# Kernel optimization log

Measured on AMD Instinct MI355X. Metric: run time of the kernel, lower is better.

## Reference

```python
import jax, jax.numpy as jnp
import numpy as np

B, T, C = 2, 2048, 1024
H, D = 16, 64
EPS = 1e-05
SCALE = 1.0 / np.sqrt(D)


def _rmsnorm(x, w):
    # normalize over last dim (head_dim)
    return w * (x * jax.lax.rsqrt(jnp.mean(x * x, axis=-1, keepdims=True) + EPS))


def setup_inputs() -> dict:
    key = jax.random.key(0)
    ks = jax.random.split(key, 8)
    x = jax.random.normal(ks[0], (B, T, C), dtype=jnp.float32)
    # causal mask, 1 = attend, 0 = masked
    attention_mask = jnp.tril(jnp.ones((T, T), dtype=jnp.int32))[None, None]
    s = 1.0 / np.sqrt(C)
    Wq = jax.random.normal(ks[1], (C, H * D), dtype=jnp.float32) * s
    Wk = jax.random.normal(ks[2], (C, H * D), dtype=jnp.float32) * s
    Wv = jax.random.normal(ks[3], (C, H * D), dtype=jnp.float32) * s
    Wo = jax.random.normal(ks[4], (H * D, C), dtype=jnp.float32) * s
    q_norm_w = jnp.ones((D,), dtype=jnp.float32)
    k_norm_w = jnp.ones((D,), dtype=jnp.float32)
    gate = jnp.ones((1, H, 1, 1), dtype=jnp.float32)
    return {"x": x, "attention_mask": attention_mask, "Wq": Wq, "Wk": Wk,
            "Wv": Wv, "Wo": Wo, "q_norm_w": q_norm_w, "k_norm_w": k_norm_w,
            "gate": gate}


def reference(x, attention_mask, Wq, Wk, Wv, Wo, q_norm_w, k_norm_w, gate):
    Bx, Tx, Cx = x.shape
    vx = x @ Wv                                   # [B,T,H*D] (kept for value residual)
    q = (x @ Wq).reshape(Bx, Tx, H, D).transpose(0, 2, 1, 3)  # [B,H,T,D]
    k = (x @ Wk).reshape(Bx, Tx, H, D).transpose(0, 2, 1, 3)
    v = vx.reshape(Bx, Tx, H, D).transpose(0, 2, 1, 3)
    q = _rmsnorm(q, q_norm_w)
    k = _rmsnorm(k, k_norm_w)
    att = jnp.einsum('bhqd,bhkd->bhqk', q, k) * SCALE
    att = jnp.where(attention_mask == 0, -jnp.inf, att)
    att = jax.nn.softmax(att, axis=-1)
    att = att * gate                              # per-head gating after softmax
    out = jnp.einsum('bhqk,bhkd->bhqd', att, v)
    out = out.transpose(0, 2, 1, 3).reshape(Bx, Tx, Cx)
    out = out + vx                                # value residual
    out = out @ Wo
    return out
```

## Files before the change

kernel.cpp:

```cpp
#include <hip/hip_runtime.h>

#define T_SEQ 2048
#define CDIM 1024
#define NHEAD 16
#define HDIM 64
#define BATCH 2
#define EPSV 1e-5f
#define SCALE 0.125f
#define LOG2E 1.44269504088896f
#define SMAX 16.0f

typedef __attribute__((ext_vector_type(8))) short bf16x8;
typedef __attribute__((ext_vector_type(4))) float f32x4;

__device__ __forceinline__ float b2f(short s) {
  unsigned u = ((unsigned)(unsigned short)s) << 16;
  return __builtin_bit_cast(float, u);
}
__device__ __forceinline__ short f2b(float f) {
  unsigned u = __builtin_bit_cast(unsigned, f);
  unsigned r = (u + 0x7fffu + ((u >> 16) & 1u)) >> 16;
  return (short)r;
}
__device__ __forceinline__ unsigned cvt_pk_bf16(float a, float b) {
  unsigned r;
  asm("v_cvt_pk_bf16_f32 %0, %1, %2" : "=v"(r) : "v"(a), "v"(b));
  return r;
}

__device__ __forceinline__ void gld16(const void* g, void* l) {
  __builtin_amdgcn_global_load_lds((const __attribute__((address_space(1))) unsigned*)g,
                                   (__attribute__((address_space(3))) unsigned*)l, 16, 0, 0);
}

__device__ __forceinline__ void stage_sw(short* lds, const char* gbase, int gstride,
                                         int w, int l) {
#pragma unroll
  for (int i = 0; i < 2; ++i) {
    int chunk = w * 2048 + i * 1024 + l * 16;
    int row = chunk >> 7;
    int bir = chunk & 127;
    const char* src = gbase + (size_t)row * gstride + (bir ^ ((row & 7) << 4));
    gld16(src, (char*)lds + (w * 2048 + i * 1024));
  }
}

__global__ __launch_bounds__(256) void prep(const float* __restrict__ x,
                                            const float* __restrict__ Wq,
                                            const float* __restrict__ Wk,
                                            const float* __restrict__ Wv,
                                            const float* __restrict__ Wo,
                                            short* __restrict__ xb,
                                            short* __restrict__ WT) {
  __shared__ float tile[64][65];
  const int bid = blockIdx.x;
  if (bid < 2048) {
    size_t i = ((size_t)bid * 256 + threadIdx.x) * 8;
    float4 a = *(const float4*)&x[i];
    float4 b = *(const float4*)&x[i + 4];
    short4 lo, hi;
    lo.x = f2b(a.x); lo.y = f2b(a.y); lo.z = f2b(a.z); lo.w = f2b(a.w);
    hi.x = f2b(b.x); hi.y = f2b(b.y); hi.z = f2b(b.z); hi.w = f2b(b.w);
    *(short4*)&xb[i] = lo;
    *(short4*)&xb[i + 4] = hi;
    return;
  }
  const int t = bid - 2048;
  const int z = t >> 8, rem = t & 255;
  const float* W = (z == 0) ? Wq : (z == 1) ? Wk : (z == 2) ? Wv : Wo;
  const int r0 = (rem >> 4) * 64, c0 = (rem & 15) * 64;
  const int tr = threadIdx.x >> 4, tc4 = (threadIdx.x & 15) * 4;
#pragma unroll
  for (int i = 0; i < 4; ++i) {
    float4 v = *(const float4*)&W[(size_t)(r0 + tr + i * 16) * 1024 + c0 + tc4];
    tile[tr + i * 16][tc4 + 0] = v.x;
    tile[tr + i * 16][tc4 + 1] = v.y;
    tile[tr + i * 16][tc4 + 2] = v.z;
    tile[tr + i * 16][tc4 + 3] = v.w;
  }
  __syncthreads();
#pragma unroll
  for (int i = 0; i < 4; ++i) {
    int n = tr + i * 16;
    short4 o;
    o.x = f2b(tile[tc4 + 0][n]);
    o.y = f2b(tile[tc4 + 1][n]);
    o.z = f2b(tile[tc4 + 2][n]);
    o.w = f2b(tile[tc4 + 3][n]);
    *(short4*)&WT[((size_t)(z * 1024) + c0 + n) * 1024 + r0 + tc4] = o;
  }
}

template <int BN, bool F32OUT, bool NORM, bool VTOUT>
__global__ __launch_bounds__(256) void gemm_bf16(const short* __restrict__ A,
                                                 const short* __restrict__ Bt,
                                                 void* __restrict__ Cv,
                                                 const float* __restrict__ qw,
                                                 const float* __restrict__ kw,
                                                 short* __restrict__ VTb,
                                                 int M, int N, int K) {
  constexpr int NFR = BN / 32;
  __shared__ __attribute__((aligned(16))) short As[2][128 * 32];
  __shared__ __attribute__((aligned(16))) short Bs[2][BN * 32];
  const int tid = threadIdx.x;
  const int w = tid >> 6, l = tid & 63;
  const int g = l >> 4, c = l & 15;
  const int wm = w >> 1, wn = w & 1;
  const int m0 = blockIdx.y * 128, n0 = blockIdx.x * BN;
  const char* Ab = (const char*)A;
  const char* Bb = (const char*)Bt;

  auto stage = [&](int k0, int buf) {
#pragma unroll
    for (int i = 0; i < 2; ++i) {
      int chunk = w * 2048 + i * 1024 + l * 16;
      int row = chunk >> 6, bir = chunk & 63;
      gld16(Ab + ((size_t)(m0 + row) * K + k0) * 2 + bir,
            (char*)As[buf] + (w * 2048 + i * 1024));
    }
#pragma unroll
    for (int i = 0; i < BN / 64; ++i) {
      int chunk = w * (BN * 16) + i * 1024 + l * 16;
      int row = chunk >> 6, bir = chunk & 63;
      gld16(Bb + ((size_t)(n0 + row) * K + k0) * 2 + bir,
            (char*)Bs[buf] + (w * (BN * 16) + i * 1024));
    }
  };

  f32x4 acc[4][NFR];
#pragma unroll
  for (int mt = 0; mt < 4; ++mt)
#pragma unroll
    for (int nt = 0; nt < NFR; ++nt) {
      f32x4 z = {0.f, 0.f, 0.f, 0.f};
      acc[mt][nt] = z;
    }

  stage(0, 0);
  __syncthreads();
  int cur = 0;
  for (int k0 = 0; k0 < K; k0 += 32) {
    if (k0 + 32 < K) stage(k0 + 32, cur ^ 1);
    bf16x8 a[4], bf[NFR];
#pragma unroll
    for (int mt = 0; mt < 4; ++mt)
      a[mt] = *(const bf16x8*)&As[cur][(wm * 64 + mt * 16 + c) * 32 + g * 8];
#pragma unroll
    for (int nt = 0; nt < NFR; ++nt)
      bf[nt] = *(const bf16x8*)&Bs[cur][(wn * (BN / 2) + nt * 16 + c) * 32 + g * 8];
#pragma unroll
    for (int mt = 0; mt < 4; ++mt)
#pragma unroll
      for (int nt = 0; nt < NFR; ++nt)
        acc[mt][nt] = __builtin_amdgcn_mfma_f32_16x16x32_bf16(a[mt], bf[nt], acc[mt][nt], 0, 0, 0);
    __syncthreads();
    cur ^= 1;
  }

  if constexpr (NORM) {
    if (n0 < 2048) {
      const float* wgt = (n0 < 1024) ? qw : kw;
      const float scl = (n0 < 1024) ? SCALE * LOG2E : 1.f;
      float w4[NFR];
#pragma unroll
      for (int nt = 0; nt < NFR; ++nt) w4[nt] = wgt[nt * 16 + c] * scl;
#pragma unroll
      for (int mt = 0; mt < 4; ++mt)
#pragma unroll
        for (int r = 0; r < 4; ++r) {
          float s = 0.f;
#pragma unroll
          for (int nt = 0; nt < NFR; ++nt) s += acc[mt][nt][r] * acc[mt][nt][r];
          s += __shfl_xor(s, 1);
          s += __shfl_xor(s, 2);
          s += __shfl_xor(s, 4);
          s += __shfl_xor(s, 8);
          const float rstd = rsqrtf(s * (1.0f / 64.0f) + EPSV);
#pragma unroll
          for (int nt = 0; nt < NFR; ++nt) acc[mt][nt][r] *= rstd * w4[nt];
        }
    }
  }

  if constexpr (VTOUT) {
    if (n0 >= 2048) {
      const int bb = m0 >> 11;
      const int tbase = (m0 & 2047) + wm * 64 + 4 * g;
#pragma unroll
      for (int nt = 0; nt < NFR; ++nt) {
        const int cv = n0 - 2048 + wn * (BN / 2) + nt * 16 + c;
        short* dst = VTb + ((size_t)(bb * 1024 + cv)) * T_SEQ;
#pragma unroll
        for (int mt = 0; mt < 4; ++mt) {
          short4 o;
          o.x = f2b(acc[mt][nt][0]);
          o.y = f2b(acc[mt][nt][1]);
          o.z = f2b(acc[mt][nt][2]);
          o.w = f2b(acc[mt][nt][3]);
          *(short4*)&dst[tbase + mt * 16] = o;
        }
      }
    }
  }

  if constexpr (F32OUT) {
    float* C = (float*)Cv;
#pragma unroll
    for (int mt = 0; mt < 4; ++mt)
#pragma unroll
      for (int nt = 0; nt < NFR; ++nt)
#pragma unroll
        for (int r = 0; r < 4; ++r)
          C[(size_t)(m0 + wm * 64 + mt * 16 + 4 * g + r) * N + n0 + wn * (BN / 2) + nt * 16 + c] =
              acc[mt][nt][r];
  } else {
    short* C = (short*)Cv;
#pragma unroll
    for (int mt = 0; mt < 4; ++mt)
#pragma unroll
      for (int nt = 0; nt < NFR; ++nt)
#pragma unroll
        for (int r = 0; r < 4; ++r)
          C[(size_t)(m0 + wm * 64 + mt * 16 + 4 * g + r) * N + n0 + wn * (BN / 2) + nt * 16 + c] =
              f2b(acc[mt][nt][r]);
  }
}

__global__ __launch_bounds__(256) void attn_fwd(const short* __restrict__ QKV,
                                                const short* __restrict__ VT,
                                                const float* __restrict__ gate,
                                                short* __restrict__ Ob) {
  __shared__ __attribute__((aligned(16))) short pool[20480];
  short* Qs = pool;
  short* Ksb = pool + 4096;
  short* Vsb = pool + 12288;

  const int bid = blockIdx.x;
  const int xcd = bid & 7, s = bid >> 3;
  const int a = s & 31, bq = s >> 5, k4 = a >> 2;
  const int qt = (bq == 0) ? 31 - k4 : (bq == 1) ? k4 : (bq == 2) ? 23 - k4 : 8 + k4;
  const int bh = xcd * 4 + (a & 3);
  const int h = bh & 15, b = bh >> 4;
  const int q0 = qt * 64;
  const int tid = threadIdx.x;
  const int w = tid >> 6, l = tid & 63;
  const int g = l >> 4, c = l & 15;

  const char* qkb = (const char*)QKV;
  const char* kbase = qkb + ((size_t)(b * T_SEQ) * 3072 + 1024 + h * 64) * 2;
  const char* vtb = (const char*)VT + ((size_t)(b * NHEAD + h) * 64) * T_SEQ * 2;
  const float gh = gate[h];

  stage_sw(Qs, qkb + ((size_t)(b * T_SEQ + q0) * 3072 + h * 64) * 2, 3072 * 2, w, l);
  stage_sw(Ksb, kbase, 3072 * 2, w, l);
  stage_sw(Vsb, vtb, T_SEQ * 2, w, l);
  __syncthreads();

  bf16x8 qf[2];
  {
    const int row = w * 16 + c;
#pragma unroll
    for (int ks = 0; ks < 2; ++ks)
      qf[ks] = *(const bf16x8*)&Qs[row * 64 + ((ks * 32 + g * 8) ^ ((row & 7) << 3))];
  }
  short* ps = pool + (w << 10);

  f32x4 oacc[4];
#pragma unroll
  for (int dt = 0; dt < 4; ++dt) {
    f32x4 z = {0.f, 0.f, 0.f, 0.f};
    oacc[dt] = z;
  }
  float lpart = 0.f;
  int cur = 0;

  for (int kt = 0; kt <= qt; ++kt) {
    if (kt < qt) {
      stage_sw(Ksb + ((cur ^ 1) << 12), kbase + (size_t)(kt + 1) * 64 * 3072 * 2, 3072 * 2, w, l);
      stage_sw(Vsb + ((cur ^ 1) << 12), vtb + (size_t)(kt + 1) * 64 * 2, T_SEQ * 2, w, l);
    }
    f32x4 sacc[4];
#pragma unroll
    for (int mt = 0; mt < 4; ++mt) {
      f32x4 z = {-SMAX, -SMAX, -SMAX, -SMAX};
      sacc[mt] = z;
    }
    __builtin_amdgcn_s_setprio(1);
#pragma unroll
    for (int mt = 0; mt < 4; ++mt) {
      const int row = mt * 16 + c;
#pragma unroll
      for (int ks = 0; ks < 2; ++ks) {
        bf16x8 kf = *(const bf16x8*)&Ksb[(cur << 12) + row * 64 + ((ks * 32 + g * 8) ^ ((row & 7) << 3))];
        sacc[mt] = __builtin_amdgcn_mfma_f32_16x16x32_bf16(kf, qf[ks], sacc[mt], 0, 0, 0);
      }
    }
    __builtin_amdgcn_s_setprio(0);
    bf16x8 vf[4][2];
#pragma unroll
    for (int dt = 0; dt < 4; ++dt) {
      const int row = dt * 16 + c;
#pragma unroll
      for (int ks = 0; ks < 2; ++ks)
        vf[dt][ks] = *(const bf16x8*)&Vsb[(cur << 12) + row * 64 + ((ks * 32 + g * 8) ^ ((row & 7) << 3))];
    }
    if (kt == qt) {
#pragma unroll
      for (int mt = 0; mt < 4; ++mt)
#pragma unroll
        for (int r = 0; r < 4; ++r)
          if (mt * 16 + 4 * g + r > w * 16 + c) sacc[mt][r] = -1e30f;
    }
#pragma unroll
    for (int mt = 0; mt < 4; ++mt) {
      float p0 = exp2f(sacc[mt][0]);
      float p1 = exp2f(sacc[mt][1]);
      float p2 = exp2f(sacc[mt][2]);
      float p3 = exp2f(sacc[mt][3]);
      lpart += (p0 + p1) + (p2 + p3);
      uint2 pk;
      pk.x = cvt_pk_bf16(p0, p1);
      pk.y = cvt_pk_bf16(p2, p3);
      *(uint2*)&ps[(c << 6) + ((mt * 16 + 4 * g) ^ ((c & 7) << 3))] = pk;
    }
    bf16x8 pb[2];
#pragma unroll
    for (int ks = 0; ks < 2; ++ks)
      pb[ks] = *(const bf16x8*)&ps[(c << 6) + ((ks * 32 + g * 8) ^ ((c & 7) << 3))];
    __builtin_amdgcn_s_setprio(1);
#pragma unroll
    for (int dt = 0; dt < 4; ++dt)
#pragma unroll
      for (int ks = 0; ks < 2; ++ks)
        oacc[dt] = __builtin_amdgcn_mfma_f32_16x16x32_bf16(vf[dt][ks], pb[ks], oacc[dt], 0, 0, 0);
    __builtin_amdgcn_s_setprio(0);
    __syncthreads();
    cur ^= 1;
  }
  float lsum = lpart;
  lsum += __shfl_xor(lsum, 16);
  lsum += __shfl_xor(lsum, 32);
  const float gl = gh / lsum;
  const short* Vr = QKV + (size_t)(b * T_SEQ + q0 + w * 16 + c) * 3072 + 2048 + h * 64;
  short* Oro = Ob + (size_t)(b * T_SEQ + q0 + w * 16 + c) * 1024 + h * 64;
#pragma unroll
  for (int dt = 0; dt < 4; ++dt) {
    const int d0 = dt * 16 + 4 * g;
    short4 vres = *(const short4*)&Vr[d0];
    short4 o;
    o.x = f2b(oacc[dt][0] * gl + b2f(vres.x));
    o.y = f2b(oacc[dt][1] * gl + b2f(vres.y));
    o.z = f2b(oacc[dt][2] * gl + b2f(vres.z));
    o.w = f2b(oacc[dt][3] * gl + b2f(vres.w));
    *(short4*)&Oro[d0] = o;
  }
}

extern "C" void kernel_launch(void* const* d_in, const int* in_sizes, int n_in,
                              void* d_out, int out_size, void* d_ws, size_t ws_size,
                              hipStream_t stream) {
  const float* x  = (const float*)d_in[0];
  const float* Wq = (const float*)d_in[2];
  const float* Wk = (const float*)d_in[3];
  const float* Wv = (const float*)d_in[4];
  const float* Wo = (const float*)d_in[5];
  const float* qw = (const float*)d_in[6];
  const float* kw = (const float*)d_in[7];
  const float* gate = (const float*)d_in[8];
  float* out = (float*)d_out;

  char* ws = (char*)d_ws;
  short* xb  = (short*)ws;
  short* WT  = (short*)(ws + ((size_t)8 << 20));
  short* QKV = (short*)(ws + ((size_t)16 << 20));
  short* VTb = (short*)(ws + ((size_t)40 << 20));
  short* Obf = (short*)(ws + ((size_t)48 << 20));

  const int M = BATCH * T_SEQ;

  prep<<<3072, 256, 0, stream>>>(x, Wq, Wk, Wv, Wo, xb, WT);
  gemm_bf16<128, false, true, true><<<dim3(24, 32), 256, 0, stream>>>(
      xb, WT, QKV, qw, kw, VTb, M, 3072, CDIM);
  attn_fwd<<<1024, 256, 0, stream>>>(QKV, VTb, gate, Obf);
  gemm_bf16<128, true, false, false><<<dim3(8, 32), 256, 0, stream>>>(
      Obf, WT + (size_t)3072 * 1024, out, nullptr, nullptr, nullptr, M, CDIM, CDIM);
}
```

Measured before the change: 126.4 us.

## Triple-buffer GEMM with swizzled LDS, XCD-aware block remap, separate V transpose

The bf16 GEMM moves from double to triple buffering of LDS tiles, using vmcnt-based waits and one barrier per k-step so global loads run two tiles ahead. It adds an XOR swizzle to the LDS layout to reduce bank conflicts, remaps block IDs so neighbouring tiles land on the same XCD for better L2 reuse, and raises wave priority around the MFMA block. The fused transposed-V store in the QKV GEMM epilogue is replaced by a separate vt_kernel that transposes V through shared memory. That adds one launch and an extra read and write of V in exchange for a simpler epilogue with fewer scattered stores.

```diff
diff --git a/kernel.cpp b/kernel.cpp
--- a/kernel.cpp
+++ b/kernel.cpp
@@ -91,115 +91,112 @@
   }
 }
 
-template <int BN, bool F32OUT, bool NORM, bool VTOUT>
+template <bool F32OUT, bool NORM>
 __global__ __launch_bounds__(256) void gemm_bf16(const short* __restrict__ A,
                                                  const short* __restrict__ Bt,
                                                  void* __restrict__ Cv,
                                                  const float* __restrict__ qw,
                                                  const float* __restrict__ kw,
-                                                 short* __restrict__ VTb,
-                                                 int M, int N, int K) {
-  constexpr int NFR = BN / 32;
-  __shared__ __attribute__((aligned(16))) short As[2][128 * 32];
-  __shared__ __attribute__((aligned(16))) short Bs[2][BN * 32];
+                                                 int M, int N, int K, int nbx) {
+  __shared__ __attribute__((aligned(16))) short As[3][4096];
+  __shared__ __attribute__((aligned(16))) short Bs[3][4096];
   const int tid = threadIdx.x;
   const int w = tid >> 6, l = tid & 63;
   const int g = l >> 4, c = l & 15;
   const int wm = w >> 1, wn = w & 1;
-  const int m0 = blockIdx.y * 128, n0 = blockIdx.x * BN;
+  const int cpx = gridDim.x >> 3;
+  const int wg = (blockIdx.x & 7) * cpx + (blockIdx.x >> 3);
+  const int bx = wg % nbx, by = wg / nbx;
+  const int m0 = by * 128, n0 = bx * 128;
   const char* Ab = (const char*)A;
   const char* Bb = (const char*)Bt;
 
   auto stage = [&](int k0, int buf) {
 #pragma unroll
     for (int i = 0; i < 2; ++i) {
-      int chunk = w * 2048 + i * 1024 + l * 16;
-      int row = chunk >> 6, bir = chunk & 63;
-      gld16(Ab + ((size_t)(m0 + row) * K + k0) * 2 + bir,
+      int ci = w * 128 + i * 64 + l;
+      int row = ci >> 2, c4 = ci & 3;
+      gld16(Ab + ((size_t)(m0 + row) * K + k0) * 2 + ((c4 ^ (row & 3)) << 4),
             (char*)As[buf] + (w * 2048 + i * 1024));
     }
 #pragma unroll
-    for (int i = 0; i < BN / 64; ++i) {
-      int chunk = w * (BN * 16) + i * 1024 + l * 16;
-      int row = chunk >> 6, bir = chunk & 63;
-      gld16(Bb + ((size_t)(n0 + row) * K + k0) * 2 + bir,
-            (char*)Bs[buf] + (w * (BN * 16) + i * 1024));
+    for (int i = 0; i < 2; ++i) {
+      int ci = w * 128 + i * 64 + l;
+      int row = ci >> 2, c4 = ci & 3;
+      gld16(Bb + ((size_t)(n0 + row) * K + k0) * 2 + ((c4 ^ (row & 3)) << 4),
+            (char*)Bs[buf] + (w * 2048 + i * 1024));
     }
   };
 
-  f32x4 acc[4][NFR];
+  f32x4 acc[4][4];
 #pragma unroll
   for (int mt = 0; mt < 4; ++mt)
 #pragma unroll
-    for (int nt = 0; nt < NFR; ++nt) {
+    for (int nt = 0; nt < 4; ++nt) {
       f32x4 z = {0.f, 0.f, 0.f, 0.f};
       acc[mt][nt] = z;
     }
 
+  const int NT = K >> 5;
   stage(0, 0);
-  __syncthreads();
-  int cur = 0;
-  for (int k0 = 0; k0 < K; k0 += 32) {
-    if (k0 + 32 < K) stage(k0 + 32, cur ^ 1);
-    bf16x8 a[4], bf[NFR];
+  stage(32, 1);
+  asm volatile("s_waitcnt vmcnt(4)" ::: "memory");
+  __builtin_amdgcn_s_barrier();
+  __builtin_amdgcn_sched_barrier(0);
+
+  int cbuf = 0;
+  for (int t = 0; t < NT; ++t) {
+    int tgt = cbuf + 2; if (tgt >= 3) tgt -= 3;
+    if (t + 2 < NT) stage((t + 2) << 5, tgt);
+    bf16x8 a[4], bf[4];
+#pragma unroll
+    for (int mt = 0; mt < 4; ++mt) {
+      const int row = wm * 64 + mt * 16 + c;
+      a[mt] = *(const bf16x8*)&As[cbuf][row * 32 + ((g ^ (row & 3)) << 3)];
+    }
+#pragma unroll
+    for (int nt = 0; nt < 4; ++nt) {
+      const int row = wn * 64 + nt * 16 + c;
+      bf[nt] = *(const bf16x8*)&Bs[cbuf][row * 32 + ((g ^ (row & 3)) << 3)];
+    }
+    __builtin_amdgcn_s_setprio(1);
 #pragma unroll
     for (int mt = 0; mt < 4; ++mt)
-      a[mt] = *(const bf16x8*)&As[cur][(wm * 64 + mt * 16 + c) * 32 + g * 8];
-#pragma unroll
-    for (int nt = 0; nt < NFR; ++nt)
-      bf[nt] = *(const bf16x8*)&Bs[cur][(wn * (BN / 2) + nt * 16 + c) * 32 + g * 8];
-#pragma unroll
-    for (int mt = 0; mt < 4; ++mt)
-#pragma unroll
-      for (int nt = 0; nt < NFR; ++nt)
+#pragma unroll
+      for (int nt = 0; nt < 4; ++nt)
         acc[mt][nt] = __builtin_amdgcn_mfma_f32_16x16x32_bf16(a[mt], bf[nt], acc[mt][nt], 0, 0, 0);
-    __syncthreads();
-    cur ^= 1;
+    __builtin_amdgcn_s_setprio(0);
+    if (t + 1 < NT) {
+      if (t + 2 < NT) asm volatile("s_waitcnt vmcnt(4)" ::: "memory");
+      else            asm volatile("s_waitcnt vmcnt(0)" ::: "memory");
+      __builtin_amdgcn_s_barrier();
+      __builtin_amdgcn_sched_barrier(0);
+    }
+    cbuf = cbuf + 1; if (cbuf >= 3) cbuf -= 3;
   }
 
   if constexpr (NORM) {
     if (n0 < 2048) {
       const float* wgt = (n0 < 1024) ? qw : kw;
       const float scl = (n0 < 1024) ? SCALE * LOG2E : 1.f;
-      float w4[NFR];
-#pragma unroll
-      for (int nt = 0; nt < NFR; ++nt) w4[nt] = wgt[nt * 16 + c] * scl;
+      float w4[4];
+#pragma unroll
+      for (int nt = 0; nt < 4; ++nt) w4[nt] = wgt[nt * 16 + c] * scl;
 #pragma unroll
       for (int mt = 0; mt < 4; ++mt)
 #pragma unroll
         for (int r = 0; r < 4; ++r) {
           float s = 0.f;
 #pragma unroll
-          for (int nt = 0; nt < NFR; ++nt) s += acc[mt][nt][r] * acc[mt][nt][r];
+          for (int nt = 0; nt < 4; ++nt) s += acc[mt][nt][r] * acc[mt][nt][r];
           s += __shfl_xor(s, 1);
           s += __shfl_xor(s, 2);
           s += __shfl_xor(s, 4);
           s += __shfl_xor(s, 8);
           const float rstd = rsqrtf(s * (1.0f / 64.0f) + EPSV);
 #pragma unroll
-          for (int nt = 0; nt < NFR; ++nt) acc[mt][nt][r] *= rstd * w4[nt];
+          for (int nt = 0; nt < 4; ++nt) acc[mt][nt][r] *= rstd * w4[nt];
         }
-    }
-  }
-
-  if constexpr (VTOUT) {
-    if (n0 >= 2048) {
-      const int bb = m0 >> 11;
-      const int tbase = (m0 & 2047) + wm * 64 + 4 * g;
-#pragma unroll
-      for (int nt = 0; nt < NFR; ++nt) {
-        const int cv = n0 - 2048 + wn * (BN / 2) + nt * 16 + c;
-        short* dst = VTb + ((size_t)(bb * 1024 + cv)) * T_SEQ;
-#pragma unroll
-        for (int mt = 0; mt < 4; ++mt) {
-          short4 o;
-          o.x = f2b(acc[mt][nt][0]);
-          o.y = f2b(acc[mt][nt][1]);
-          o.z = f2b(acc[mt][nt][2]);
-          o.w = f2b(acc[mt][nt][3]);
-          *(short4*)&dst[tbase + mt * 16] = o;
-        }
-      }
     }
   }
 
@@ -208,21 +205,46 @@
 #pragma unroll
     for (int mt = 0; mt < 4; ++mt)
 #pragma unroll
-      for (int nt = 0; nt < NFR; ++nt)
+      for (int nt = 0; nt < 4; ++nt)
 #pragma unroll
         for (int r = 0; r < 4; ++r)
-          C[(size_t)(m0 + wm * 64 + mt * 16 + 4 * g + r) * N + n0 + wn * (BN / 2) + nt * 16 + c] =
+          C[(size_t)(m0 + wm * 64 + mt * 16 + 4 * g + r) * N + n0 + wn * 64 + nt * 16 + c] =
               acc[mt][nt][r];
   } else {
     short* C = (short*)Cv;
 #pragma unroll
     for (int mt = 0; mt < 4; ++mt)
 #pragma unroll
-      for (int nt = 0; nt < NFR; ++nt)
+      for (int nt = 0; nt < 4; ++nt)
 #pragma unroll
         for (int r = 0; r < 4; ++r)
-          C[(size_t)(m0 + wm * 64 + mt * 16 + 4 * g + r) * N + n0 + wn * (BN / 2) + nt * 16 + c] =
+          C[(size_t)(m0 + wm * 64 + mt * 16 + 4 * g + r) * N + n0 + wn * 64 + nt * 16 + c] =
               f2b(acc[mt][nt][r]);
+  }
+}
+
+__global__ __launch_bounds__(256) void vt_kernel(const short* __restrict__ QKV,
+                                                 short* __restrict__ VT) {
+  __shared__ short tile[64][66];
+  const int t0 = blockIdx.x * 64;
+  const int h = blockIdx.y, b = blockIdx.z;
+  const int tid = threadIdx.x;
+  const int r = tid >> 3, c8 = (tid & 7) * 8;
+#pragma unroll
+  for (int p = 0; p < 2; ++p) {
+    int row = r + p * 32;
+    bf16x8 v = *(const bf16x8*)&QKV[(size_t)(b * T_SEQ + t0 + row) * 3072 + 2048 + h * 64 + c8];
+#pragma unroll
+    for (int j = 0; j < 8; ++j) tile[row][c8 + j] = v[j];
+  }
+  __syncthreads();
+#pragma unroll
+  for (int p = 0; p < 2; ++p) {
+    int d = r + p * 32;
+    short o[8];
+#pragma unroll
+    for (int j = 0; j < 8; ++j) o[j] = tile[c8 + j][d];
+    *(bf16x8*)&VT[((size_t)(b * NHEAD + h) * 64 + d) * T_SEQ + t0 + c8] = *(bf16x8*)o;
   }
 }
 
@@ -379,9 +401,9 @@
   const int M = BATCH * T_SEQ;
 
   prep<<<3072, 256, 0, stream>>>(x, Wq, Wk, Wv, Wo, xb, WT);
-  gemm_bf16<128, false, true, true><<<dim3(24, 32), 256, 0, stream>>>(
-      xb, WT, QKV, qw, kw, VTb, M, 3072, CDIM);
+  gemm_bf16<false, true><<<768, 256, 0, stream>>>(xb, WT, QKV, qw, kw, M, 3072, CDIM, 24);
+  vt_kernel<<<dim3(32, 16, 2), 256, 0, stream>>>(QKV, VTb);
   attn_fwd<<<1024, 256, 0, stream>>>(QKV, VTb, gate, Obf);
-  gemm_bf16<128, true, false, false><<<dim3(8, 32), 256, 0, stream>>>(
-      Obf, WT + (size_t)3072 * 1024, out, nullptr, nullptr, nullptr, M, CDIM, CDIM);
-}
+  gemm_bf16<true, false><<<256, 256, 0, stream>>>(Obf, WT + (size_t)3072 * 1024, out,
+                                                  nullptr, nullptr, M, CDIM, CDIM, 8);
+}
```

Result: faster. 117.0 us (-7.4%).
